# Performance work log

Measured on AMD Instinct MI355X. Metric: run time of the kernel, lower is better.

## Reference

```python
import jax, jax.numpy as jnp
import numpy as np

DIM = 512
D = 256
SCALE = D ** (-0.5)


def setup_inputs() -> dict:
    key = jax.random.key(0)
    ks = jax.random.split(key, 7)
    B, N, K = 16, 4096, 32
    g = 0.1 * (6.0 / (DIM + D)) ** 0.5  # xavier_uniform with gain=0.1
    return {
        "E_patches": jax.random.normal(ks[0], (B, N, DIM), jnp.float32),
        "T_b5": jax.random.normal(ks[1], (B, K, DIM), jnp.float32),
        "P_batch": jax.random.uniform(ks[2], (B, N), jnp.float32),
        "Wq": jax.random.uniform(ks[3], (D, DIM), jnp.float32, -g, g),
        "Wk": jax.random.uniform(ks[4], (D, DIM), jnp.float32, -g, g),
        "Wv": jax.random.uniform(ks[5], (D, DIM), jnp.float32, -g, g),
        "Wo": jax.random.uniform(ks[6], (DIM, D), jnp.float32, -g, g),
    }


def reference(E_patches, T_b5, P_batch, Wq, Wk, Wv, Wo):
    # Projections (torch Linear: x @ W.T)
    Q = jnp.einsum('bkm,dm->bkd', T_b5, Wq)       # [B,K,D]
    Kp = jnp.einsum('bnm,dm->bnd', E_patches, Wk)  # [B,N,D]
    V = jnp.einsum('bnm,dm->bnd', E_patches, Wv)   # [B,N,D]
    scores = jnp.einsum('bkd,bnd->bkn', Q, Kp) * SCALE
    logP = jnp.log(jnp.clip(P_batch, 0.1, 0.9))    # [B,N]
    scores = scores + logP[:, None, :]             # additive log-prior bias
    A = jax.nn.softmax(scores, axis=-1)            # [B,K,N]
    F_agg = jnp.einsum('bkn,bnd->bkd', A, V)
    F_agg = jnp.einsum('bkd,md->bkm', F_agg, Wo)   # [B,K,DIM]
    F_agg = F_agg / (jnp.linalg.norm(F_agg, axis=-1, keepdims=True) + 1e-8)
    return (F_agg, A)
```

## Files before the change

kernel.cpp:

```cpp
#include <hip/hip_runtime.h>

typedef __bf16 bf16x8 __attribute__((ext_vector_type(8)));
typedef __bf16 bf16x4 __attribute__((ext_vector_type(4)));
typedef float  f32x4  __attribute__((ext_vector_type(4)));

__device__ __forceinline__ void cp16(void* lds, const void* g) {
  __builtin_amdgcn_global_load_lds(
      (const __attribute__((address_space(1))) unsigned int*)g,
      (__attribute__((address_space(3))) unsigned int*)lds, 16, 0, 0);
}

#define VMCNT0 asm volatile("s_waitcnt vmcnt(0)" ::: "memory")
#define LGKM0  asm volatile("s_waitcnt lgkmcnt(0)" ::: "memory")
#define BARRAW __builtin_amdgcn_s_barrier
#define MFMA   __builtin_amdgcn_mfma_f32_16x16x32_bf16


__global__ __launch_bounds__(256) void cvt_small(const float* __restrict__ Wq,
                                                 const float* __restrict__ Wk,
                                                 const float* __restrict__ Wv,
                                                 const float* __restrict__ T,
                                                 __bf16* __restrict__ Wqb,
                                                 __bf16* __restrict__ Tbf,
                                                 __bf16* __restrict__ WkT,
                                                 float* __restrict__ WvT) {
  const int idx = blockIdx.x * 256 + threadIdx.x;
  if (idx < 32768) {
    const int o = idx * 4;
    f32x4 v = *(const f32x4*)(Wq + o);
    bf16x4 b;
    b[0] = (__bf16)v[0]; b[1] = (__bf16)v[1];
    b[2] = (__bf16)v[2]; b[3] = (__bf16)v[3];
    *(bf16x4*)(Wqb + o) = b;
  } else if (idx < 98304) {
    const int o = (idx - 32768) * 4;
    f32x4 v = *(const f32x4*)(T + o);
    bf16x4 b;
    b[0] = (__bf16)v[0]; b[1] = (__bf16)v[1];
    b[2] = (__bf16)v[2]; b[3] = (__bf16)v[3];
    *(bf16x4*)(Tbf + o) = b;
  } else if (idx < 106496) {
    const int t2 = idx - 98304;
    const int d0 = (t2 >> 7) * 4, m0 = (t2 & 127) * 4;
    f32x4 r0 = *(const f32x4*)(Wk + (size_t)(d0 + 0) * 512 + m0);
    f32x4 r1 = *(const f32x4*)(Wk + (size_t)(d0 + 1) * 512 + m0);
    f32x4 r2 = *(const f32x4*)(Wk + (size_t)(d0 + 2) * 512 + m0);
    f32x4 r3 = *(const f32x4*)(Wk + (size_t)(d0 + 3) * 512 + m0);
#pragma unroll
    for (int j = 0; j < 4; ++j) {
      bf16x4 o;
      o[0] = (__bf16)r0[j]; o[1] = (__bf16)r1[j];
      o[2] = (__bf16)r2[j]; o[3] = (__bf16)r3[j];
      *(bf16x4*)(WkT + (size_t)(m0 + j) * 256 + d0) = o;
    }
  } else {
    const int t2 = idx - 106496;
    const int d0 = (t2 >> 7) * 4, m0 = (t2 & 127) * 4;
    f32x4 r0 = *(const f32x4*)(Wv + (size_t)(d0 + 0) * 512 + m0);
    f32x4 r1 = *(const f32x4*)(Wv + (size_t)(d0 + 1) * 512 + m0);
    f32x4 r2 = *(const f32x4*)(Wv + (size_t)(d0 + 2) * 512 + m0);
    f32x4 r3 = *(const f32x4*)(Wv + (size_t)(d0 + 3) * 512 + m0);
#pragma unroll
    for (int j = 0; j < 4; ++j) {
      f32x4 o;
      o[0] = r0[j]; o[1] = r1[j]; o[2] = r2[j]; o[3] = r3[j];
      *(f32x4*)(WvT + (size_t)(m0 + j) * 256 + d0) = o;
    }
  }
}

__global__ __launch_bounds__(256) void qproj(const __bf16* __restrict__ Wqb,
                                             const __bf16* __restrict__ Tbf,
                                             __bf16* __restrict__ Qw) {
  __shared__ __align__(16) __bf16 At[4096];
  __shared__ __align__(16) __bf16 Bt[4096];
  const int tid = threadIdx.x, lane = tid & 63;
  const int q = lane >> 4, ln = lane & 15;
  const int w = tid >> 6, wm = w >> 1, wn = w & 1;
  const int t = blockIdx.x;
  const int nbase = (t & 3) * 128;
  const int mbase = (t >> 2) * 128;
  f32x4 acc[4][4] = {};
  for (int kt = 0; kt < 16; ++kt) {
    const int k0 = kt * 32;
    __syncthreads();
#pragma unroll
    for (int s = 0; s < 2; ++s) {
      const int cbase = (tid & 192) + s * 256;
      const int cc = cbase + lane;
      const int row = cc >> 2, kc = (cc & 3) * 8;
      cp16(&At[cbase * 8], Wqb + (size_t)(mbase + row) * 512 + k0 + kc);
      cp16(&Bt[cbase * 8], Tbf + (size_t)(nbase + row) * 512 + k0 + kc);
    }
    __syncthreads();
    bf16x8 af[4], bfr[4];
#pragma unroll
    for (int f = 0; f < 4; ++f) {
      af[f]  = *(const bf16x8*)&At[(wm * 64 + f * 16 + ln) * 32 + q * 8];
      bfr[f] = *(const bf16x8*)&Bt[(wn * 64 + f * 16 + ln) * 32 + q * 8];
    }
#pragma unroll
    for (int fm = 0; fm < 4; ++fm)
#pragma unroll
      for (int fn = 0; fn < 4; ++fn)
        acc[fm][fn] = MFMA(af[fm], bfr[fn], acc[fm][fn], 0, 0, 0);
  }
#pragma unroll
  for (int fm = 0; fm < 4; ++fm)
#pragma unroll
    for (int fn = 0; fn < 4; ++fn) {
      const int m = mbase + wm * 64 + fm * 16 + q * 4;
      const int n = nbase + wn * 64 + fn * 16 + ln;
      f32x4 v = acc[fm][fn];
      bf16x4 o;
      o[0] = (__bf16)v[0]; o[1] = (__bf16)v[1];
      o[2] = (__bf16)v[2]; o[3] = (__bf16)v[3];
      *(bf16x4*)&Qw[(size_t)n * 256 + m] = o;
    }
}

__global__ __launch_bounds__(256) void qwk(const __bf16* __restrict__ WkT,
                                           const __bf16* __restrict__ Qwp,
                                           __bf16* __restrict__ QWkb) {
  __shared__ __align__(16) __bf16 At[4096];
  __shared__ __align__(16) __bf16 Bt[4096];
  const int tid = threadIdx.x, lane = tid & 63;
  const int q = lane >> 4, ln = lane & 15;
  const int w = tid >> 6, wm = w >> 1, wn = w & 1;
  const int t = blockIdx.x;
  const int nbase = (t & 3) * 128;
  const int mbase = (t >> 2) * 128;
  f32x4 acc[4][4] = {};
  for (int kt = 0; kt < 8; ++kt) {
    const int k0 = kt * 32;
    __syncthreads();
#pragma unroll
    for (int s = 0; s < 2; ++s) {
      const int cbase = (tid & 192) + s * 256;
      const int cc = cbase + lane;
      const int row = cc >> 2, kc = (cc & 3) * 8;
      cp16(&At[cbase * 8], WkT + (size_t)(mbase + row) * 256 + k0 + kc);
      cp16(&Bt[cbase * 8], Qwp + (size_t)(nbase + row) * 256 + k0 + kc);
    }
    __syncthreads();
    bf16x8 af[4], bfr[4];
#pragma unroll
    for (int f = 0; f < 4; ++f) {
      af[f]  = *(const bf16x8*)&At[(wm * 64 + f * 16 + ln) * 32 + q * 8];
      bfr[f] = *(const bf16x8*)&Bt[(wn * 64 + f * 16 + ln) * 32 + q * 8];
    }
#pragma unroll
    for (int fm = 0; fm < 4; ++fm)
#pragma unroll
      for (int fn = 0; fn < 4; ++fn)
        acc[fm][fn] = MFMA(af[fm], bfr[fn], acc[fm][fn], 0, 0, 0);
  }
#pragma unroll
  for (int fm = 0; fm < 4; ++fm)
#pragma unroll
    for (int fn = 0; fn < 4; ++fn) {
      const int m = mbase + wm * 64 + fm * 16 + q * 4;
      const int n = nbase + wn * 64 + fn * 16 + ln;
      f32x4 v = acc[fm][fn];
      bf16x4 o;
      o[0] = (__bf16)v[0]; o[1] = (__bf16)v[1];
      o[2] = (__bf16)v[2]; o[3] = (__bf16)v[3];
      *(bf16x4*)&QWkb[(size_t)n * 512 + m] = o;
    }
}

__device__ __forceinline__ void load_e(f32x4 (&ev)[16], const float* Eb,
                                       int s, int rg, int cg0) {
#pragma unroll
  for (int i = 0; i < 4; ++i) {
    const int cg = cg0 + i * 32;
#pragma unroll
    for (int r = 0; r < 4; ++r)
      ev[i * 4 + r] = *(const f32x4*)(Eb + (size_t)(s * 64 + rg * 4 + r) * 512 + cg * 4);
  }
}
__device__ __forceinline__ void cvtwrite_e(const f32x4 (&ev)[16], __bf16* Er,
                                           __bf16* EtT, int rg, int cg0) {
#pragma unroll
  for (int i = 0; i < 4; ++i) {
    const int cg = cg0 + i * 32;
#pragma unroll
    for (int r = 0; r < 4; ++r) {
      bf16x4 rw;
      rw[0] = (__bf16)ev[i*4+r][0]; rw[1] = (__bf16)ev[i*4+r][1];
      rw[2] = (__bf16)ev[i*4+r][2]; rw[3] = (__bf16)ev[i*4+r][3];
      *(bf16x4*)((char*)Er + (size_t)(rg * 4 + r) * 1040 + cg * 8) = rw;
    }
#pragma unroll
    for (int j = 0; j < 4; ++j) {
      bf16x4 tw;
      tw[0] = (__bf16)ev[i*4+0][j]; tw[1] = (__bf16)ev[i*4+1][j];
      tw[2] = (__bf16)ev[i*4+2][j]; tw[3] = (__bf16)ev[i*4+3][j];
      const int m = cg * 4 + j;
      const int u = (rg >> 1) ^ ((m >> 3) & 7);
      *(bf16x4*)((char*)EtT + (size_t)m * 144 + u * 16 + (rg & 1) * 8) = tw;
    }
  }
}

__global__ __launch_bounds__(512, 2) void fused_main(
    const float* __restrict__ E, const __bf16* __restrict__ QWkb,
    const float* __restrict__ Pb, __bf16* __restrict__ Pws,
    float* __restrict__ Fpart, float* __restrict__ rowsum) {
  __shared__ __align__(16) __bf16 Er[64 * 520];
  __shared__ __align__(16) __bf16 EtT[512 * 72];
  __shared__ __align__(16) __bf16 Plds[32 * 72];
  __shared__ __align__(16) float Lp[256];
  __shared__ float rsum[32];

  const int tid = threadIdx.x;
  const int lane = tid & 63;
  const int q = lane >> 4, ln = lane & 15;
  const int w = tid >> 6;
  const int kf = w >> 2;
  const int nf = w & 3;
  const int b = blockIdx.y, c = blockIdx.x;
  const int rg = tid >> 5;
  const int cg0 = tid & 31;

  const float* Eb = E + ((size_t)b * 4096 + (size_t)c * 256) * 512;

  bf16x8 qf[16];
  {
    const __bf16* qr = QWkb + (size_t)(b * 32 + kf * 16 + ln) * 512 + q * 8;
#pragma unroll
    for (int kk = 0; kk < 16; ++kk) qf[kk] = *(const bf16x8*)(qr + kk * 32);
  }
  if (tid < 256) {
    float p = Pb[b * 4096 + c * 256 + tid];
    Lp[tid] = __logf(fminf(fmaxf(p, 0.1f), 0.9f));
  }
  if (tid < 32) rsum[tid] = 0.f;

  f32x4 ev[16];
  load_e(ev, Eb, 0, rg, cg0);
  VMCNT0;
  cvtwrite_e(ev, Er, EtT, rg, cg0);
  load_e(ev, Eb, 1, rg, cg0);
  LGKM0; BARRAW();

  f32x4 facc[2][4] = {};
  for (int s = 0; s < 4; ++s) {
    f32x4 sacc = {0.f, 0.f, 0.f, 0.f};
#pragma unroll
    for (int kk = 0; kk < 16; ++kk) {
      bf16x8 bb = *(const bf16x8*)((char*)Er + (size_t)(nf * 16 + ln) * 1040 + kk * 64 + q * 16);
      sacc = MFMA(qf[kk], bb, sacc, 0, 0, 0);
    }
    const float lp = Lp[s * 64 + nf * 16 + ln];
    float pv[4];
#pragma unroll
    for (int r = 0; r < 4; ++r) {
      pv[r] = __expf(sacc[r] * 0.0625f + lp);
      Plds[(kf * 16 + q * 4 + r) * 72 + nf * 16 + ln] = (__bf16)pv[r];
    }
#pragma unroll
    for (int mm = 1; mm < 16; mm <<= 1)
#pragma unroll
      for (int r = 0; r < 4; ++r) pv[r] += __shfl_xor(pv[r], mm, 64);
    if (ln == 0) {
#pragma unroll
      for (int r = 0; r < 4; ++r) atomicAdd(&rsum[kf * 16 + q * 4 + r], pv[r]);
    }
    LGKM0; BARRAW();
#pragma unroll
    for (int kkn = 0; kkn < 2; ++kkn) {
      bf16x8 pa0 = *(const bf16x8*)((char*)Plds + (size_t)(ln) * 144 + kkn * 64 + q * 16);
      bf16x8 pa1 = *(const bf16x8*)((char*)Plds + (size_t)(16 + ln) * 144 + kkn * 64 + q * 16);
#pragma unroll
      for (int mf = 0; mf < 4; ++mf) {
        const int m = w * 64 + mf * 16 + ln;
        const int u = (kkn * 4 + q) ^ ((m >> 3) & 7);
        bf16x8 vb = *(const bf16x8*)((char*)EtT + (size_t)m * 144 + u * 16);
        facc[0][mf] = MFMA(pa0, vb, facc[0][mf], 0, 0, 0);
        facc[1][mf] = MFMA(pa1, vb, facc[1][mf], 0, 0, 0);
      }
    }
    {
      const int k = tid >> 4, j = (tid & 15) * 4;
      bf16x4 pc = *(const bf16x4*)((char*)Plds + (size_t)k * 144 + j * 2);
      *(bf16x4*)(Pws + (size_t)(b * 32 + k) * 4096 + c * 256 + s * 64 + j) = pc;
    }
    BARRAW();
    if (s < 3) {
      VMCNT0;
      cvtwrite_e(ev, Er, EtT, rg, cg0);
      if (s < 2) load_e(ev, Eb, s + 2, rg, cg0);
      LGKM0; BARRAW();
    }
  }
  float* Fp = Fpart + ((size_t)c * 512 + b * 32) * 512;
#pragma unroll
  for (int kf2 = 0; kf2 < 2; ++kf2)
#pragma unroll
    for (int mf = 0; mf < 4; ++mf)
#pragma unroll
      for (int r = 0; r < 4; ++r)
        Fp[(size_t)(kf2 * 16 + q * 4 + r) * 512 + w * 64 + mf * 16 + ln] = facc[kf2][mf][r];
  if (tid < 32) atomicAdd(&rowsum[b * 32 + tid], rsum[tid]);
}

__global__ __launch_bounds__(256) void norm_p(const __bf16* __restrict__ Pws,
                                              const float* __restrict__ rowsum,
                                              float* __restrict__ Aout) {
  const size_t idx = ((size_t)blockIdx.x * 256 + threadIdx.x) * 4;
  const int row = (int)(idx >> 12);
  const float invs = 1.0f / rowsum[row];
  bf16x4 p = *(const bf16x4*)(Pws + idx);
  f32x4 o;
  o[0] = (float)p[0] * invs; o[1] = (float)p[1] * invs;
  o[2] = (float)p[2] * invs; o[3] = (float)p[3] * invs;
  *(f32x4*)(Aout + idx) = o;
}

__global__ __launch_bounds__(256) void final_kernel(const float* __restrict__ Fpart,
                                                    const float* __restrict__ WvT,
                                                    const float* __restrict__ Wo,
                                                    float* __restrict__ Fout) {
  __shared__ float fl[512];
  __shared__ float agg[256];
  __shared__ float redbuf[4];
  const int row = blockIdx.x;
  const int t = threadIdx.x;
  float s0 = 0.f, s1 = 0.f;
#pragma unroll
  for (int cc = 0; cc < 16; ++cc) {
    const float* p = Fpart + (size_t)cc * 262144 + (size_t)row * 512;
    s0 += p[t]; s1 += p[t + 256];
  }
  fl[t] = s0; fl[t + 256] = s1;
  __syncthreads();
  float a0 = 0.f, a1 = 0.f, a2 = 0.f, a3 = 0.f;
  for (int m = 0; m < 512; m += 4) {
    a0 += fl[m]     * WvT[(size_t)m * 256 + t];
    a1 += fl[m + 1] * WvT[(size_t)(m + 1) * 256 + t];
    a2 += fl[m + 2] * WvT[(size_t)(m + 2) * 256 + t];
    a3 += fl[m + 3] * WvT[(size_t)(m + 3) * 256 + t];
  }
  agg[t] = (a0 + a1) + (a2 + a3);
  __syncthreads();
  float f2[2];
#pragma unroll
  for (int h = 0; h < 2; ++h) {
    const float* wr = Wo + (size_t)(t + h * 256) * 256;
    float d0 = 0.f, d1 = 0.f, d2 = 0.f, d3 = 0.f;
    for (int d = 0; d < 256; d += 4) {
      f32x4 wv = *(const f32x4*)(wr + d);
      d0 += wv[0] * agg[d];     d1 += wv[1] * agg[d + 1];
      d2 += wv[2] * agg[d + 2]; d3 += wv[3] * agg[d + 3];
    }
    f2[h] = (d0 + d1) + (d2 + d3);
  }
  float ps = f2[0] * f2[0] + f2[1] * f2[1];
#pragma unroll
  for (int m = 1; m < 64; m <<= 1) ps += __shfl_xor(ps, m, 64);
  if ((t & 63) == 0) redbuf[t >> 6] = ps;
  __syncthreads();
  const float tot = redbuf[0] + redbuf[1] + redbuf[2] + redbuf[3];
  const float sc = 1.0f / (sqrtf(tot) + 1e-8f);
  Fout[(size_t)row * 512 + t] = f2[0] * sc;
  Fout[(size_t)row * 512 + t + 256] = f2[1] * sc;
}

extern "C" void kernel_launch(void* const* d_in, const int* in_sizes, int n_in,
                              void* d_out, int out_size, void* d_ws, size_t ws_size,
                              hipStream_t stream) {
  const float* E  = (const float*)d_in[0];
  const float* T  = (const float*)d_in[1];
  const float* Pb = (const float*)d_in[2];
  const float* Wq = (const float*)d_in[3];
  const float* Wk = (const float*)d_in[4];
  const float* Wv = (const float*)d_in[5];
  const float* Wo = (const float*)d_in[6];

  float* out  = (float*)d_out;
  float* Fout = out;
  float* Aout = out + 262144;

  char* ws = (char*)d_ws;
  float*  Fpart = (float*)ws;
  __bf16* Pws   = (__bf16*)(ws + 16777216);
  __bf16* Tbf   = (__bf16*)(ws + 20971520);
  __bf16* Wqb   = (__bf16*)(ws + 21495808);
  __bf16* WkT   = (__bf16*)(ws + 21757952);
  float*  WvT   = (float*)(ws + 22020096);
  __bf16* Qw    = (__bf16*)(ws + 22544384);
  __bf16* QWkb  = (__bf16*)(ws + 22806528);
  float*  rowsum = (float*)(ws + 23330816);

  hipMemsetAsync(rowsum, 0, 2048, stream);

  cvt_small<<<448, 256, 0, stream>>>(Wq, Wk, Wv, T, Wqb, Tbf, WkT, WvT);
  qproj<<<8, 256, 0, stream>>>(Wqb, Tbf, Qw);
  qwk<<<16, 256, 0, stream>>>(WkT, Qw, QWkb);
  fused_main<<<dim3(16, 16), 512, 0, stream>>>(E, QWkb, Pb, Pws, Fpart, rowsum);
  norm_p<<<2048, 256, 0, stream>>>(Pws, rowsum, Aout);
  final_kernel<<<512, 256, 0, stream>>>(Fpart, WvT, Wo, Fout);
}
```

Baseline: 300.1 us.

## Double-buffer E register prefetch, defer P stores, merge tail kernels

The main loop is fully unrolled and uses two register buffers for E tiles, so two tile loads are in flight and the code waits with a partial vmcnt instead of draining all loads. The bf16 probability stores to the workspace are deferred to the end of the kernel, keeping them out of the wait counts in the pipeline. The normalisation kernel and the final projection kernel are merged into one launch with block-index dispatch, which removes one launch. The extra 64 registers per thread for the second buffer risk spills or lower occupancy under launch_bounds(512,2).

```diff
diff --git a/kernel.cpp b/kernel.cpp
--- a/kernel.cpp
+++ b/kernel.cpp
@@ -10,10 +10,11 @@
       (__attribute__((address_space(3))) unsigned int*)lds, 16, 0, 0);
 }
 
-#define VMCNT0 asm volatile("s_waitcnt vmcnt(0)" ::: "memory")
-#define LGKM0  asm volatile("s_waitcnt lgkmcnt(0)" ::: "memory")
-#define BARRAW __builtin_amdgcn_s_barrier
-#define MFMA   __builtin_amdgcn_mfma_f32_16x16x32_bf16
+#define VMCNT16 asm volatile("s_waitcnt vmcnt(16)" ::: "memory")
+#define VMCNT0  asm volatile("s_waitcnt vmcnt(0)" ::: "memory")
+#define LGKM0   asm volatile("s_waitcnt lgkmcnt(0)" ::: "memory")
+#define BARRAW  __builtin_amdgcn_s_barrier
+#define MFMA    __builtin_amdgcn_mfma_f32_16x16x32_bf16
 
 
 __global__ __launch_bounds__(256) void cvt_small(const float* __restrict__ Wq,
@@ -202,6 +203,50 @@
     }
   }
 }
+__device__ __forceinline__ void phase1(int s, const bf16x8 (&qf)[16],
+                                       const __bf16* Er, __bf16* Plds,
+                                       const float* Lp, float* rsum,
+                                       int kf, int nf, int q, int ln) {
+  f32x4 sacc = {0.f, 0.f, 0.f, 0.f};
+#pragma unroll
+  for (int kk = 0; kk < 16; ++kk) {
+    bf16x8 bb = *(const bf16x8*)((char*)Er + (size_t)(nf * 16 + ln) * 1040 + kk * 64 + q * 16);
+    sacc = MFMA(qf[kk], bb, sacc, 0, 0, 0);
+  }
+  const float lp = Lp[s * 64 + nf * 16 + ln];
+  float pv[4];
+#pragma unroll
+  for (int r = 0; r < 4; ++r) {
+    pv[r] = __expf(sacc[r] * 0.0625f + lp);
+    Plds[(kf * 16 + q * 4 + r) * 72 + nf * 16 + ln] = (__bf16)pv[r];
+  }
+#pragma unroll
+  for (int mm = 1; mm < 16; mm <<= 1)
+#pragma unroll
+    for (int r = 0; r < 4; ++r) pv[r] += __shfl_xor(pv[r], mm, 64);
+  if (ln == 0) {
+#pragma unroll
+    for (int r = 0; r < 4; ++r) atomicAdd(&rsum[kf * 16 + q * 4 + r], pv[r]);
+  }
+}
+__device__ __forceinline__ void phase2a(f32x4 (&facc)[2][4], const __bf16* Plds,
+                                        const __bf16* EtT, int w, int q, int ln,
+                                        int tid, bf16x4* pr) {
+#pragma unroll
+  for (int kkn = 0; kkn < 2; ++kkn) {
+    bf16x8 pa0 = *(const bf16x8*)((char*)Plds + (size_t)(ln) * 144 + kkn * 64 + q * 16);
+    bf16x8 pa1 = *(const bf16x8*)((char*)Plds + (size_t)(16 + ln) * 144 + kkn * 64 + q * 16);
+#pragma unroll
+    for (int mf = 0; mf < 4; ++mf) {
+      const int m = w * 64 + mf * 16 + ln;
+      const int u = (kkn * 4 + q) ^ ((m >> 3) & 7);
+      bf16x8 vb = *(const bf16x8*)((char*)EtT + (size_t)m * 144 + u * 16);
+      facc[0][mf] = MFMA(pa0, vb, facc[0][mf], 0, 0, 0);
+      facc[1][mf] = MFMA(pa1, vb, facc[1][mf], 0, 0, 0);
+    }
+  }
+  *pr = *(const bf16x4*)((char*)Plds + (size_t)(tid >> 4) * 144 + (tid & 15) * 8);
+}
 
 __global__ __launch_bounds__(512, 2) void fused_main(
     const float* __restrict__ E, const __bf16* __restrict__ QWkb,
@@ -237,62 +282,50 @@
   }
   if (tid < 32) rsum[tid] = 0.f;
 
-  f32x4 ev[16];
-  load_e(ev, Eb, 0, rg, cg0);
+  f32x4 evA[16], evB[16];
+  load_e(evA, Eb, 0, rg, cg0);
+  load_e(evB, Eb, 1, rg, cg0);
+  VMCNT16;
+  cvtwrite_e(evA, Er, EtT, rg, cg0);
+  load_e(evA, Eb, 2, rg, cg0);
+  LGKM0; BARRAW();
+
+  f32x4 facc[2][4] = {};
+  bf16x4 pr0, pr1, pr2, pr3;
+
+  phase1(0, qf, Er, Plds, Lp, rsum, kf, nf, q, ln);
+  LGKM0; BARRAW();
+  phase2a(facc, Plds, EtT, w, q, ln, tid, &pr0);
+  BARRAW();
+  VMCNT16;
+  cvtwrite_e(evB, Er, EtT, rg, cg0);
+  load_e(evB, Eb, 3, rg, cg0);
+  LGKM0; BARRAW();
+  phase1(1, qf, Er, Plds, Lp, rsum, kf, nf, q, ln);
+  LGKM0; BARRAW();
+  phase2a(facc, Plds, EtT, w, q, ln, tid, &pr1);
+  BARRAW();
+  VMCNT16;
+  cvtwrite_e(evA, Er, EtT, rg, cg0);
+  LGKM0; BARRAW();
+  phase1(2, qf, Er, Plds, Lp, rsum, kf, nf, q, ln);
+  LGKM0; BARRAW();
+  phase2a(facc, Plds, EtT, w, q, ln, tid, &pr2);
+  BARRAW();
   VMCNT0;
-  cvtwrite_e(ev, Er, EtT, rg, cg0);
-  load_e(ev, Eb, 1, rg, cg0);
-  LGKM0; BARRAW();
-
-  f32x4 facc[2][4] = {};
-  for (int s = 0; s < 4; ++s) {
-    f32x4 sacc = {0.f, 0.f, 0.f, 0.f};
-#pragma unroll
-    for (int kk = 0; kk < 16; ++kk) {
-      bf16x8 bb = *(const bf16x8*)((char*)Er + (size_t)(nf * 16 + ln) * 1040 + kk * 64 + q * 16);
-      sacc = MFMA(qf[kk], bb, sacc, 0, 0, 0);
-    }
-    const float lp = Lp[s * 64 + nf * 16 + ln];
-    float pv[4];
-#pragma unroll
-    for (int r = 0; r < 4; ++r) {
-      pv[r] = __expf(sacc[r] * 0.0625f + lp);
-      Plds[(kf * 16 + q * 4 + r) * 72 + nf * 16 + ln] = (__bf16)pv[r];
-    }
-#pragma unroll
-    for (int mm = 1; mm < 16; mm <<= 1)
-#pragma unroll
-      for (int r = 0; r < 4; ++r) pv[r] += __shfl_xor(pv[r], mm, 64);
-    if (ln == 0) {
-#pragma unroll
-      for (int r = 0; r < 4; ++r) atomicAdd(&rsum[kf * 16 + q * 4 + r], pv[r]);
-    }
-    LGKM0; BARRAW();
-#pragma unroll
-    for (int kkn = 0; kkn < 2; ++kkn) {
-      bf16x8 pa0 = *(const bf16x8*)((char*)Plds + (size_t)(ln) * 144 + kkn * 64 + q * 16);
-      bf16x8 pa1 = *(const bf16x8*)((char*)Plds + (size_t)(16 + ln) * 144 + kkn * 64 + q * 16);
-#pragma unroll
-      for (int mf = 0; mf < 4; ++mf) {
-        const int m = w * 64 + mf * 16 + ln;
-        const int u = (kkn * 4 + q) ^ ((m >> 3) & 7);
-        bf16x8 vb = *(const bf16x8*)((char*)EtT + (size_t)m * 144 + u * 16);
-        facc[0][mf] = MFMA(pa0, vb, facc[0][mf], 0, 0, 0);
-        facc[1][mf] = MFMA(pa1, vb, facc[1][mf], 0, 0, 0);
-      }
-    }
-    {
-      const int k = tid >> 4, j = (tid & 15) * 4;
-      bf16x4 pc = *(const bf16x4*)((char*)Plds + (size_t)k * 144 + j * 2);
-      *(bf16x4*)(Pws + (size_t)(b * 32 + k) * 4096 + c * 256 + s * 64 + j) = pc;
-    }
-    BARRAW();
-    if (s < 3) {
-      VMCNT0;
-      cvtwrite_e(ev, Er, EtT, rg, cg0);
-      if (s < 2) load_e(ev, Eb, s + 2, rg, cg0);
-      LGKM0; BARRAW();
-    }
+  cvtwrite_e(evB, Er, EtT, rg, cg0);
+  LGKM0; BARRAW();
+  phase1(3, qf, Er, Plds, Lp, rsum, kf, nf, q, ln);
+  LGKM0; BARRAW();
+  phase2a(facc, Plds, EtT, w, q, ln, tid, &pr3);
+
+  {
+    const int k = tid >> 4, j = (tid & 15) * 4;
+    __bf16* pwr = Pws + (size_t)(b * 32 + k) * 4096 + c * 256 + j;
+    *(bf16x4*)(pwr)       = pr0;
+    *(bf16x4*)(pwr + 64)  = pr1;
+    *(bf16x4*)(pwr + 128) = pr2;
+    *(bf16x4*)(pwr + 192) = pr3;
   }
   float* Fp = Fpart + ((size_t)c * 512 + b * 32) * 512;
 #pragma unroll
@@ -305,28 +338,28 @@
   if (tid < 32) atomicAdd(&rowsum[b * 32 + tid], rsum[tid]);
 }
 
-__global__ __launch_bounds__(256) void norm_p(const __bf16* __restrict__ Pws,
-                                              const float* __restrict__ rowsum,
-                                              float* __restrict__ Aout) {
-  const size_t idx = ((size_t)blockIdx.x * 256 + threadIdx.x) * 4;
-  const int row = (int)(idx >> 12);
-  const float invs = 1.0f / rowsum[row];
-  bf16x4 p = *(const bf16x4*)(Pws + idx);
-  f32x4 o;
-  o[0] = (float)p[0] * invs; o[1] = (float)p[1] * invs;
-  o[2] = (float)p[2] * invs; o[3] = (float)p[3] * invs;
-  *(f32x4*)(Aout + idx) = o;
-}
-
-__global__ __launch_bounds__(256) void final_kernel(const float* __restrict__ Fpart,
-                                                    const float* __restrict__ WvT,
-                                                    const float* __restrict__ Wo,
-                                                    float* __restrict__ Fout) {
+__global__ __launch_bounds__(256) void tail_kernel(
+    const __bf16* __restrict__ Pws, const float* __restrict__ rowsum,
+    float* __restrict__ Aout, const float* __restrict__ Fpart,
+    const float* __restrict__ WvT, const float* __restrict__ Wo,
+    float* __restrict__ Fout) {
   __shared__ float fl[512];
   __shared__ float agg[256];
   __shared__ float redbuf[4];
-  const int row = blockIdx.x;
+  const int bid = blockIdx.x;
   const int t = threadIdx.x;
+  if (bid < 2048) {
+    const size_t idx = ((size_t)bid * 256 + t) * 4;
+    const int row = (int)(idx >> 12);
+    const float invs = 1.0f / rowsum[row];
+    bf16x4 p = *(const bf16x4*)(Pws + idx);
+    f32x4 o;
+    o[0] = (float)p[0] * invs; o[1] = (float)p[1] * invs;
+    o[2] = (float)p[2] * invs; o[3] = (float)p[3] * invs;
+    *(f32x4*)(Aout + idx) = o;
+    return;
+  }
+  const int row = bid - 2048;
   float s0 = 0.f, s1 = 0.f;
 #pragma unroll
   for (int cc = 0; cc < 16; ++cc) {
@@ -399,6 +432,5 @@
   qproj<<<8, 256, 0, stream>>>(Wqb, Tbf, Qw);
   qwk<<<16, 256, 0, stream>>>(WkT, Qw, QWkb);
   fused_main<<<dim3(16, 16), 512, 0, stream>>>(E, QWkb, Pb, Pws, Fpart, rowsum);
-  norm_p<<<2048, 256, 0, stream>>>(Pws, rowsum, Aout);
-  final_kernel<<<512, 256, 0, stream>>>(Fpart, WvT, Wo, Fout);
-}
+  tail_kernel<<<2560, 256, 0, stream>>>(Pws, rowsum, Aout, Fpart, WvT, Wo, Fout);
+}
```

Result: slower. 341.9 us (+13.9%).
